# Kernel optimization log

Hardware: AMD Instinct MI355X
Metric: run time of the kernel (lower is better)

## Reference

```python
import jax, jax.numpy as jnp
import numpy as np

H, D = 8, 16
HD = H * D
SCALE0 = float(1.0 / np.sqrt(D * 1))   # degree-0 dot-product scale (order m=1)
SCALE1 = float(1.0 / np.sqrt(D * 3))   # degree-1 dot-product scale (order m=3)
SHARED = float(np.sqrt(0.5))           # shared_scale = sqrt(1/2) for DOT_PROD + SHARED
NEG = -1e9


def _split_heads_q(x):  # (b,n,HD,m) -> (b,H,n,D,m)
    b, n, _, m = x.shape
    return x.reshape(b, n, H, D, m).transpose(0, 2, 1, 3, 4)


def _split_heads_k(x):  # (b,n,N,HD,m) -> (b,H,n,N,D,m)
    b, n, N, _, m = x.shape
    return x.reshape(b, n, N, H, D, m).transpose(0, 3, 1, 2, 4, 5)


def _augment_kv(k, v, feats, W_self, null_k, null_v):
    # attend_self: VNLinear self key/value; use_null_kv: learned null tokens.
    b, n = feats.shape[:2]
    m = feats.shape[-1]
    skv = jnp.einsum('oc,bncm->bnom', W_self, feats)          # (b,n,2HD,m)
    sk, sv = jnp.split(skv, 2, axis=-2)
    sk = _split_heads_q(sk)[:, :, :, None]                     # (b,H,n,1,D,m)
    sv = _split_heads_q(sv)[:, :, :, None]
    nk = jnp.broadcast_to(null_k[None, :, None, None], (b, H, n, 1, D, m))
    nv = jnp.broadcast_to(null_v[None, :, None, None], (b, H, n, 1, D, m))
    k = jnp.concatenate([nk, sk, k], axis=3)                   # (b,H,n,2+N,D,m)
    v = jnp.concatenate([nv, sv, v], axis=3)
    return k, v


def _merge_heads(x):  # (b,H,n,D,m) -> (b,n,HD,m)
    b, _, n, _, m = x.shape
    return x.transpose(0, 2, 1, 3, 4).reshape(b, n, HD, m)


def _forward(q0, k0, v0, q1, k1, v1, feats0, feats1, edges,
             W_self_kv0, W_self_kv1, W_bias, self_bias, null_bias,
             null_k0, null_v0, null_k1, null_v1, head_weights1,
             W_out0, W_out1, neighbor_mask):
    b, n, N = edges.shape[:3]
    q0h, k0h, v0h = _split_heads_q(q0), _split_heads_k(k0), _split_heads_k(v0)
    q1h, k1h, v1h = _split_heads_q(q1), _split_heads_k(k1), _split_heads_k(v1)
    k0h, v0h = _augment_kv(k0h, v0h, feats0, W_self_kv0, null_k0, null_v0)
    k1h, v1h = _augment_kv(k1h, v1h, feats1, W_self_kv1, null_k1, null_v1)

    # pair bias for degree 0 (to_order==1); prepend null/self bias columns
    edge_bias = jnp.einsum('bnje,he->bhnj', edges, W_bias)     # (b,H,n,N)
    nb = jnp.broadcast_to(null_bias[None, :, None, None], (b, H, n, 1))
    sb = jnp.broadcast_to(self_bias[None, :, None, None], (b, H, n, 1))
    bias = jnp.concatenate([nb, sb, edge_bias], axis=-1)        # (b,H,n,2+N)

    sim0 = jnp.einsum('bhndm,bhnjdm->bhnj', q0h, k0h) * SCALE0 + bias
    w1 = jax.nn.softplus(head_weights1)                         # (1,H,1,1)
    sim1 = jnp.einsum('bhndm,bhnjdm->bhnj', q1h, k1h) * (SCALE1 * w1)

    total = (sim0 + sim1) * SHARED
    mask = jnp.concatenate(
        [jnp.ones((b, 1, n, 2), dtype=bool),                    # null + self always valid
         neighbor_mask[:, None]], axis=-1)
    total = jnp.where(mask, total, NEG)
    attn = jax.nn.softmax(total, axis=-1)                       # shared across degrees

    out0 = _merge_heads(jnp.einsum('bhnj,bhnjdm->bhndm', attn, v0h))
    out1 = _merge_heads(jnp.einsum('bhnj,bhnjdm->bhndm', attn, v1h))

    y0 = jnp.einsum('oc,bncm->bnom', W_out0, out0)              # FiberLinear deg 0
    y1 = jnp.einsum('oc,bncm->bnom', W_out1, out1)              # FiberLinear deg 1
    return y0, y1


def setup_inputs() -> dict:
    key = jax.random.key(0)
    ks = jax.random.split(key, 20)
    b, n, N, e = 1, 2048, 32, 32
    d0, d1 = 128, 64
    f = lambda k, s: jax.random.normal(k, s, dtype=jnp.float32) * 0.1
    return {
        'q0': f(ks[0], (b, n, HD, 1)), 'k0': f(ks[1], (b, n, N, HD, 1)), 'v0': f(ks[2], (b, n, N, HD, 1)),
        'q1': f(ks[3], (b, n, HD, 3)), 'k1': f(ks[4], (b, n, N, HD, 3)), 'v1': f(ks[5], (b, n, N, HD, 3)),
        'feats0': f(ks[6], (b, n, d0, 1)), 'feats1': f(ks[7], (b, n, d1, 3)),
        'edges': f(ks[8], (b, n, N, e)),
        'W_self_kv0': f(ks[9], (2 * HD, d0)), 'W_self_kv1': f(ks[10], (2 * HD, d1)),
        'W_bias': f(ks[11], (H, e)),
        'self_bias': jnp.zeros((H,), jnp.float32), 'null_bias': jnp.zeros((H,), jnp.float32),
        'null_k0': jnp.zeros((H, D, 1), jnp.float32), 'null_v0': jnp.zeros((H, D, 1), jnp.float32),
        'null_k1': jnp.zeros((H, D, 3), jnp.float32), 'null_v1': jnp.zeros((H, D, 3), jnp.float32),
        'head_weights1': jnp.full((1, H, 1, 1), float(np.log(np.e - 1.0)), jnp.float32),
        'W_out0': f(ks[12], (d0, HD)), 'W_out1': f(ks[13], (d1, HD)),
        'neighbor_mask': jax.random.uniform(ks[14], (b, n, N)) > 0.1,
    }


def reference(q0, k0, v0, q1, k1, v1, feats0, feats1, edges,
              W_self_kv0, W_self_kv1, W_bias, self_bias, null_bias,
              null_k0, null_v0, null_k1, null_v1, head_weights1,
              W_out0, W_out1, neighbor_mask):
    return _forward(q0, k0, v0, q1, k1, v1, feats0, feats1, edges,
                    W_self_kv0, W_self_kv1, W_bias, self_bias, null_bias,
                    null_k0, null_v0, null_k1, null_v1, head_weights1,
                    W_out0, W_out1, neighbor_mask)
```

## Files before the change

### kernel.cpp

```cpp
#include <hip/hip_runtime.h>

constexpr int kH  = 8;
constexpr int kD  = 16;
constexpr int kHD = 128;
constexpr int kN  = 32;
constexpr int kE  = 32;
constexpr int kD0 = 128;
constexpr int kD1 = 64;

constexpr float SCALE0   = 0.25f;
constexpr float SCALE1   = 0.14433756729740643f;
constexpr float SHARED_S = 0.70710678118654752f;
constexpr float NEGV     = -1e9f;

__global__ __launch_bounds__(256, 4) void se3_fused(
    const float* __restrict__ q0, const float* __restrict__ q1,
    const float* __restrict__ k0, const float* __restrict__ k1,
    const float* __restrict__ v0, const float* __restrict__ v1,
    const float* __restrict__ feats0, const float* __restrict__ feats1,
    const float* __restrict__ edges,
    const float* __restrict__ Wskv0, const float* __restrict__ Wskv1,
    const float* __restrict__ Wbias,
    const float* __restrict__ sbias, const float* __restrict__ nbias,
    const float* __restrict__ nk0, const float* __restrict__ nk1,
    const float* __restrict__ nv0, const float* __restrict__ nv1,
    const float* __restrict__ hw1,
    const float* __restrict__ Wout0, const float* __restrict__ Wout1,
    const int* __restrict__ nmask,
    float* __restrict__ out, int n_total)
{
  const int i = blockIdx.x;
  const int t = threadIdx.x;
  const int q4 = t & 3;
  const int qg = t >> 2;
  const int hB = qg & 7;
  const int jl = qg >> 3;

  __shared__ __align__(16) float f0s[kD0];
  __shared__ __align__(16) float f1s[kD1 * 3];
  __shared__ __align__(16) float q0s[kHD];
  __shared__ __align__(16) float q1s[kHD * 3];
  __shared__ float edg[kN * (kE + 1)];
  __shared__ float wbs[kH * kE];
  __shared__ float w1s[kH];
  __shared__ int   nmL[kN];
  __shared__ float biasL[kH][kN];
  __shared__ float sk0[kHD];
  __shared__ __align__(16) float sk1[kHD * 3];
  __shared__ __align__(16) float sv0[kHD];
  __shared__ __align__(16) float sv1[kHD * 3];
  __shared__ float sc[kH][36];
  __shared__ __align__(16) float o0p[2][kHD];
  __shared__ __align__(16) float o1p[2][kHD * 3];

  if (t < 32) {
    ((float4*)f0s)[t] = ((const float4*)(feats0 + (size_t)i * kD0))[t];
  } else if (t < 80) {
    ((float4*)f1s)[t - 32] = ((const float4*)(feats1 + (size_t)i * kD1 * 3))[t - 32];
  } else if (t < 112) {
    ((float4*)q0s)[t - 80] = ((const float4*)(q0 + (size_t)i * kHD))[t - 80];
  } else if (t < 208) {
    ((float4*)q1s)[t - 112] = ((const float4*)(q1 + (size_t)i * kHD * 3))[t - 112];
  }
  { float4 ev = ((const float4*)(edges + (size_t)i * kN * kE))[t];
    int j = t >> 3, e4 = (t & 7) * 4;
    float* dst = &edg[j * 33 + e4];
    dst[0] = ev.x; dst[1] = ev.y; dst[2] = ev.z; dst[3] = ev.w; }
  wbs[t] = Wbias[t];
  if (t < kN) nmL[t] = nmask[(size_t)i * kN + t];
  if (t < kH) w1s[t] = log1pf(expf(hw1[t]));
  __syncthreads();

  #pragma unroll
  for (int pass = 0; pass < 4; ++pass) {
    const int r = qg + 64 * pass;
    const float4* w0r = (const float4*)(Wskv0 + (size_t)r * kD0);
    float a0 = 0.f;
    #pragma unroll
    for (int g = 0; g < 8; ++g) {
      float4 w = w0r[q4 + 4 * g]; int c = (q4 + 4 * g) * 4;
      a0 += w.x * f0s[c] + w.y * f0s[c + 1]
          + w.z * f0s[c + 2] + w.w * f0s[c + 3];
    }
    const float4* w1r = (const float4*)(Wskv1 + (size_t)r * kD1);
    float a1[3] = {};
    #pragma unroll
    for (int g = 0; g < 4; ++g) {
      float4 w = w1r[q4 + 4 * g]; int c = (q4 + 4 * g) * 4;
      float wvv[4] = {w.x, w.y, w.z, w.w};
      #pragma unroll
      for (int k = 0; k < 4; ++k) {
        const float* fp = &f1s[(c + k) * 3];
        a1[0] += wvv[k] * fp[0];
        a1[1] += wvv[k] * fp[1];
        a1[2] += wvv[k] * fp[2];
      }
    }
    a0 += __shfl_xor(a0, 1); a0 += __shfl_xor(a0, 2);
    #pragma unroll
    for (int c = 0; c < 3; ++c) {
      a1[c] += __shfl_xor(a1[c], 1);
      a1[c] += __shfl_xor(a1[c], 2);
    }
    if (q4 == 0) {
      if (r < kHD) {
        sk0[r] = a0;
        sk1[r * 3 + 0] = a1[0]; sk1[r * 3 + 1] = a1[1]; sk1[r * 3 + 2] = a1[2];
      } else {
        const int o = r - kHD;
        sv0[o] = a0;
        sv1[o * 3 + 0] = a1[0]; sv1[o * 3 + 1] = a1[1]; sv1[o * 3 + 2] = a1[2];
      }
    }
  }

  {
    const int h = t >> 5, j = t & 31;
    float b = 0.f;
    #pragma unroll
    for (int e = 0; e < kE; ++e) b += edg[j * 33 + e] * wbs[h * kE + e];
    biasL[h][j] = b;
  }
  __syncthreads();

  if (t < 16) {
    const int h = t & 7;
    const bool is_self = t >= 8;
    float s0 = 0.f, s1 = 0.f, bias;
    if (is_self) {
      #pragma unroll
      for (int d = 0; d < kD; ++d) s0 += q0s[h * kD + d] * sk0[h * kD + d];
      #pragma unroll
      for (int x = 0; x < 48; ++x) s1 += q1s[h * 48 + x] * sk1[h * 48 + x];
      bias = sbias[h];
    } else {
      #pragma unroll
      for (int d = 0; d < kD; ++d) s0 += q0s[h * kD + d] * nk0[h * kD + d];
      #pragma unroll
      for (int x = 0; x < 48; ++x) s1 += q1s[h * 48 + x] * nk1[h * 48 + x];
      bias = nbias[h];
    }
    sc[h][is_self ? 1 : 0] =
        (s0 * SCALE0 + bias + s1 * SCALE1 * w1s[h]) * SHARED_S;
  }

  {
    const float w1h = w1s[hB];
    const float4 q0f = *((const float4*)(q0s + hB * kD) + q4);
    float4 q1f[3];
    #pragma unroll
    for (int pc = 0; pc < 3; ++pc)
      q1f[pc] = *((const float4*)(q1s + hB * 48 + pc * 16) + q4);

    const float* k0base = k0 + (size_t)i * kN * kHD + hB * kD + q4 * 4;
    const float* k1base = k1 + (size_t)i * kN * kHD * 3 + hB * 48 + q4 * 4;

    #pragma unroll
    for (int half = 0; half < 2; ++half) {
      float4 kv0[2];
      float4 kv1[2][3];
      #pragma unroll
      for (int pp = 0; pp < 2; ++pp) {
        const int j = (half * 2 + pp) * 8 + jl;
        kv0[pp] = *((const float4*)(k0base + (size_t)j * kHD));
        #pragma unroll
        for (int pc = 0; pc < 3; ++pc)
          kv1[pp][pc] = *((const float4*)(k1base + (size_t)j * kHD * 3 + pc * 16));
      }
      #pragma unroll
      for (int pp = 0; pp < 2; ++pp) {
        const int j = (half * 2 + pp) * 8 + jl;
        float s0 = kv0[pp].x * q0f.x + kv0[pp].y * q0f.y
                 + kv0[pp].z * q0f.z + kv0[pp].w * q0f.w;
        float s1 = 0.f;
        #pragma unroll
        for (int pc = 0; pc < 3; ++pc)
          s1 += kv1[pp][pc].x * q1f[pc].x + kv1[pp][pc].y * q1f[pc].y
              + kv1[pp][pc].z * q1f[pc].z + kv1[pp][pc].w * q1f[pc].w;
        float part = s0 * SCALE0 + s1 * SCALE1 * w1h;
        part += __shfl_xor(part, 1);
        part += __shfl_xor(part, 2);
        if (q4 == 0)
          sc[hB][2 + j] = nmL[j] ? (part + biasL[hB][j]) * SHARED_S : NEGV;
      }
      __builtin_amdgcn_sched_barrier(0);
    }
  }
  __syncthreads();

  if (t < 128) {
    const int h = t >> 4, l = t & 15;
    float* rp = sc[h];
    float va = rp[2 + l], vb = rp[2 + l + 16];
    float mx = fmaxf(va, vb);
    #pragma unroll
    for (int off = 8; off > 0; off >>= 1) mx = fmaxf(mx, __shfl_xor(mx, off));
    float e0v = rp[0], e1v = rp[1];
    mx = fmaxf(mx, fmaxf(e0v, e1v));
    float ea = __expf(va - mx), eb = __expf(vb - mx);
    float sum = ea + eb;
    #pragma unroll
    for (int off = 8; off > 0; off >>= 1) sum += __shfl_xor(sum, off);
    float ee0 = __expf(e0v - mx), ee1 = __expf(e1v - mx);
    float inv = 1.f / (sum + ee0 + ee1);
    rp[2 + l] = ea * inv;
    rp[2 + l + 16] = eb * inv;
    if (l == 0) rp[0] = ee0 * inv;
    if (l == 1) rp[1] = ee1 * inv;
  }
  __syncthreads();

  {
    const int halfD = t >> 7;
    const int s = t & 127;
    float4 acc = {0.f, 0.f, 0.f, 0.f};
    if (s < 32) {
      const int h = s >> 2;
      const float* at = sc[h];
      if (halfD == 0) {
        float4 nv = ((const float4*)nv0)[s];
        float4 sv = ((const float4*)sv0)[s];
        acc.x = at[0] * nv.x + at[1] * sv.x;
        acc.y = at[0] * nv.y + at[1] * sv.y;
        acc.z = at[0] * nv.z + at[1] * sv.z;
        acc.w = at[0] * nv.w + at[1] * sv.w;
      }
      const float4* vp = (const float4*)(v0 + (size_t)i * kN * kHD) + s;
      float4 vbuf[8];
      #pragma unroll
      for (int gg = 0; gg < 2; ++gg) {
        const int g = halfD * 2 + gg;
        #pragma unroll
        for (int r = 0; r < 8; ++r) vbuf[r] = vp[(g * 8 + r) * 32];
        #pragma unroll
        for (int r = 0; r < 8; ++r) {
          float a = at[2 + g * 8 + r];
          acc.x += a * vbuf[r].x; acc.y += a * vbuf[r].y;
          acc.z += a * vbuf[r].z; acc.w += a * vbuf[r].w;
        }
      }
      ((float4*)o0p[halfD])[s] = acc;
    } else {
      const int s1 = s - 32;
      const int h = s1 / 12;
      const float* at = sc[h];
      if (halfD == 0) {
        float4 nv = ((const float4*)nv1)[s1];
        float4 sv = ((const float4*)sv1)[s1];
        acc.x = at[0] * nv.x + at[1] * sv.x;
        acc.y = at[0] * nv.y + at[1] * sv.y;
        acc.z = at[0] * nv.z + at[1] * sv.z;
        acc.w = at[0] * nv.w + at[1] * sv.w;
      }
      const float4* vp = (const float4*)(v1 + (size_t)i * kN * kHD * 3) + s1;
      float4 vbuf[8];
      #pragma unroll
      for (int gg = 0; gg < 2; ++gg) {
        const int g = halfD * 2 + gg;
        #pragma unroll
        for (int r = 0; r < 8; ++r) vbuf[r] = vp[(g * 8 + r) * 96];
        #pragma unroll
        for (int r = 0; r < 8; ++r) {
          float a = at[2 + g * 8 + r];
          acc.x += a * vbuf[r].x; acc.y += a * vbuf[r].y;
          acc.z += a * vbuf[r].z; acc.w += a * vbuf[r].w;
        }
      }
      ((float4*)o1p[halfD])[s1] = acc;
    }
  }
  __syncthreads();

  if (t < 128) {
    if (t < 32) {
      float4 a = ((float4*)o0p[0])[t], b = ((float4*)o0p[1])[t];
      a.x += b.x; a.y += b.y; a.z += b.z; a.w += b.w;
      ((float4*)o0p[0])[t] = a;
    } else {
      const int s1 = t - 32;
      float4 a = ((float4*)o1p[0])[s1], b = ((float4*)o1p[1])[s1];
      a.x += b.x; a.y += b.y; a.z += b.z; a.w += b.w;
      ((float4*)o1p[0])[s1] = a;
    }
  }
  __syncthreads();

  #pragma unroll
  for (int pass = 0; pass < 5; ++pass) {
    const int u = qg + 64 * pass;
    if (u < 128) {
      const float4* wr = (const float4*)(Wout0 + (size_t)u * kHD);
      float a = 0.f;
      #pragma unroll
      for (int g = 0; g < 8; ++g) {
        float4 w = wr[q4 + 4 * g]; int c = (q4 + 4 * g) * 4;
        a += w.x * o0p[0][c] + w.y * o0p[0][c + 1]
           + w.z * o0p[0][c + 2] + w.w * o0p[0][c + 3];
      }
      a += __shfl_xor(a, 1); a += __shfl_xor(a, 2);
      if (q4 == 0) out[(size_t)i * kHD + u] = a;
    } else {
      const int v2 = u - 128, o = v2 / 3, m = v2 - o * 3;
      const float4* wr = (const float4*)(Wout1 + (size_t)o * kHD);
      float a = 0.f;
      #pragma unroll
      for (int g = 0; g < 8; ++g) {
        float4 w = wr[q4 + 4 * g]; int c = (q4 + 4 * g) * 4;
        a += w.x * o1p[0][(c + 0) * 3 + m] + w.y * o1p[0][(c + 1) * 3 + m]
           + w.z * o1p[0][(c + 2) * 3 + m] + w.w * o1p[0][(c + 3) * 3 + m];
      }
      a += __shfl_xor(a, 1); a += __shfl_xor(a, 2);
      if (q4 == 0)
        out[(size_t)n_total * kHD + (size_t)i * 192 + v2] = a;
    }
  }
}

extern "C" void kernel_launch(void* const* d_in, const int* in_sizes, int n_in,
                              void* d_out, int out_size, void* d_ws, size_t ws_size,
                              hipStream_t stream) {
  const int n = in_sizes[0] / kHD;
  const float* q0     = (const float*)d_in[0];
  const float* k0     = (const float*)d_in[1];
  const float* v0     = (const float*)d_in[2];
  const float* q1     = (const float*)d_in[3];
  const float* k1     = (const float*)d_in[4];
  const float* v1     = (const float*)d_in[5];
  const float* feats0 = (const float*)d_in[6];
  const float* feats1 = (const float*)d_in[7];
  const float* edges  = (const float*)d_in[8];
  const float* Wskv0  = (const float*)d_in[9];
  const float* Wskv1  = (const float*)d_in[10];
  const float* Wbias  = (const float*)d_in[11];
  const float* sbias  = (const float*)d_in[12];
  const float* nbias  = (const float*)d_in[13];
  const float* nk0    = (const float*)d_in[14];
  const float* nv0    = (const float*)d_in[15];
  const float* nk1    = (const float*)d_in[16];
  const float* nv1    = (const float*)d_in[17];
  const float* hw1    = (const float*)d_in[18];
  const float* Wout0  = (const float*)d_in[19];
  const float* Wout1  = (const float*)d_in[20];
  const int*   nmask  = (const int*)d_in[21];

  se3_fused<<<n, 256, 0, stream>>>(
      q0, q1, k0, k1, v0, v1, feats0, feats1, edges,
      Wskv0, Wskv1, Wbias, sbias, nbias, nk0, nk1, nv0, nv1, hw1,
      Wout0, Wout1, nmask, (float*)d_out, n);
}
```

Baseline: 318.7 us.

## Stream K/V neighbor chunks into LDS with double-buffered global_load_lds

Key and value tensors are now staged in chunks of 8 neighbors straight into a double-buffered LDS area using asynchronous global-to-LDS loads. The next chunk is fetched while the current one is consumed, for both the score and the value-weighting phases. The edge-bias computation now reads edges and Wbias straight from global memory, and shared buffers are reused through a scratch region to limit LDS growth. The intent is to hide global memory latency. In exchange it adds a block barrier per chunk and a larger LDS footprint that may limit occupancy, and it relies on barriers to order the asynchronous LDS writes.

```diff
diff --git a/kernel.cpp b/kernel.cpp
--- a/kernel.cpp
+++ b/kernel.cpp
@@ -13,7 +13,25 @@
 constexpr float SHARED_S = 0.70710678118654752f;
 constexpr float NEGV     = -1e9f;
 
-__global__ __launch_bounds__(256, 4) void se3_fused(
+
+__device__ __forceinline__ void gll16(const void* g, void* l) {
+  __builtin_amdgcn_global_load_lds(
+      (const __attribute__((address_space(1))) void*)(g),
+      (__attribute__((address_space(3))) void*)(l), 16, 0, 0);
+}
+
+__device__ __forceinline__ void stage_chunk(
+    const float* p0, const float* p1, int i, int c, float* buf, int t) {
+  const char* g0 = (const char*)(p0 + (size_t)i * kN * kHD + (size_t)c * 8 * kHD) + t * 16;
+  const char* g1 = (const char*)(p1 + (size_t)i * kN * kHD * 3 + (size_t)c * 8 * kHD * 3) + t * 16;
+  char* l = (char*)buf + ((t >> 6) << 10);
+  gll16(g0, l);
+  #pragma unroll
+  for (int o = 0; o < 3; ++o)
+    gll16(g1 + o * 4096, l + 4096 + o * 4096);
+}
+
+__global__ __launch_bounds__(256, 4) void se3_stream(
     const float* __restrict__ q0, const float* __restrict__ q1,
     const float* __restrict__ k0, const float* __restrict__ k1,
     const float* __restrict__ v0, const float* __restrict__ v1,
@@ -29,29 +47,28 @@
     const int* __restrict__ nmask,
     float* __restrict__ out, int n_total)
 {
-  const int i = blockIdx.x;
-  const int t = threadIdx.x;
+  const int i  = blockIdx.x;
+  const int t  = threadIdx.x;
   const int q4 = t & 3;
   const int qg = t >> 2;
   const int hB = qg & 7;
-  const int jl = qg >> 3;
-
+  const int jj = t >> 5;
+
+  __shared__ __align__(16) float kv[2][4096];
+  __shared__ __align__(16) float scratch[1024];
   __shared__ __align__(16) float f0s[kD0];
   __shared__ __align__(16) float f1s[kD1 * 3];
-  __shared__ __align__(16) float q0s[kHD];
-  __shared__ __align__(16) float q1s[kHD * 3];
-  __shared__ float edg[kN * (kE + 1)];
-  __shared__ float wbs[kH * kE];
-  __shared__ float w1s[kH];
-  __shared__ int   nmL[kN];
-  __shared__ float biasL[kH][kN];
-  __shared__ float sk0[kHD];
-  __shared__ __align__(16) float sk1[kHD * 3];
   __shared__ __align__(16) float sv0[kHD];
   __shared__ __align__(16) float sv1[kHD * 3];
   __shared__ float sc[kH][36];
-  __shared__ __align__(16) float o0p[2][kHD];
-  __shared__ __align__(16) float o1p[2][kHD * 3];
+  __shared__ float biasL[kH][kN];
+  __shared__ float w1s[kH];
+  __shared__ int   nmL[kN];
+
+  float* q0s = scratch;
+  float* q1s = scratch + 128;
+  float* sk0 = scratch + 512;
+  float* sk1 = scratch + 640;
 
   if (t < 32) {
     ((float4*)f0s)[t] = ((const float4*)(feats0 + (size_t)i * kD0))[t];
@@ -62,14 +79,12 @@
   } else if (t < 208) {
     ((float4*)q1s)[t - 112] = ((const float4*)(q1 + (size_t)i * kHD * 3))[t - 112];
   }
-  { float4 ev = ((const float4*)(edges + (size_t)i * kN * kE))[t];
-    int j = t >> 3, e4 = (t & 7) * 4;
-    float* dst = &edg[j * 33 + e4];
-    dst[0] = ev.x; dst[1] = ev.y; dst[2] = ev.z; dst[3] = ev.w; }
-  wbs[t] = Wbias[t];
   if (t < kN) nmL[t] = nmask[(size_t)i * kN + t];
   if (t < kH) w1s[t] = log1pf(expf(hw1[t]));
   __syncthreads();
+
+  stage_chunk(k0, k1, i, 0, kv[0], t);
+  stage_chunk(k0, k1, i, 1, kv[1], t);
 
   #pragma unroll
   for (int pass = 0; pass < 4; ++pass) {
@@ -113,16 +128,20 @@
       }
     }
   }
+  __syncthreads();
 
   {
     const int h = t >> 5, j = t & 31;
+    const float4* er = (const float4*)(edges + (size_t)i * kN * kE + j * kE);
+    const float4* wr = (const float4*)(Wbias + h * kE);
     float b = 0.f;
     #pragma unroll
-    for (int e = 0; e < kE; ++e) b += edg[j * 33 + e] * wbs[h * kE + e];
+    for (int g = 0; g < 8; ++g) {
+      float4 e = er[g]; float4 w = wr[g];
+      b += e.x * w.x + e.y * w.y + e.z * w.z + e.w * w.w;
+    }
     biasL[h][j] = b;
   }
-  __syncthreads();
-
   if (t < 16) {
     const int h = t & 7;
     const bool is_self = t >= 8;
@@ -143,6 +162,7 @@
     sc[h][is_self ? 1 : 0] =
         (s0 * SCALE0 + bias + s1 * SCALE1 * w1s[h]) * SHARED_S;
   }
+  __syncthreads();
 
   {
     const float w1h = w1s[hB];
@@ -152,41 +172,36 @@
     for (int pc = 0; pc < 3; ++pc)
       q1f[pc] = *((const float4*)(q1s + hB * 48 + pc * 16) + q4);
 
-    const float* k0base = k0 + (size_t)i * kN * kHD + hB * kD + q4 * 4;
-    const float* k1base = k1 + (size_t)i * kN * kHD * 3 + hB * 48 + q4 * 4;
-
-    #pragma unroll
-    for (int half = 0; half < 2; ++half) {
-      float4 kv0[2];
-      float4 kv1[2][3];
-      #pragma unroll
-      for (int pp = 0; pp < 2; ++pp) {
-        const int j = (half * 2 + pp) * 8 + jl;
-        kv0[pp] = *((const float4*)(k0base + (size_t)j * kHD));
-        #pragma unroll
-        for (int pc = 0; pc < 3; ++pc)
-          kv1[pp][pc] = *((const float4*)(k1base + (size_t)j * kHD * 3 + pc * 16));
-      }
-      #pragma unroll
-      for (int pp = 0; pp < 2; ++pp) {
-        const int j = (half * 2 + pp) * 8 + jl;
-        float s0 = kv0[pp].x * q0f.x + kv0[pp].y * q0f.y
-                 + kv0[pp].z * q0f.z + kv0[pp].w * q0f.w;
-        float s1 = 0.f;
-        #pragma unroll
-        for (int pc = 0; pc < 3; ++pc)
-          s1 += kv1[pp][pc].x * q1f[pc].x + kv1[pp][pc].y * q1f[pc].y
-              + kv1[pp][pc].z * q1f[pc].z + kv1[pp][pc].w * q1f[pc].w;
-        float part = s0 * SCALE0 + s1 * SCALE1 * w1h;
-        part += __shfl_xor(part, 1);
-        part += __shfl_xor(part, 2);
-        if (q4 == 0)
-          sc[hB][2 + j] = nmL[j] ? (part + biasL[hB][j]) * SHARED_S : NEGV;
-      }
-      __builtin_amdgcn_sched_barrier(0);
-    }
-  }
-  __syncthreads();
+    #pragma unroll
+    for (int c = 0; c < 4; ++c) {
+      if (c >= 1) {
+        if (c < 3) stage_chunk(k0, k1, i, c + 1, kv[(c + 1) & 1], t);
+        else       stage_chunk(v0, v1, i, 0,     kv[0],           t);
+      }
+      const float* kb = kv[c & 1];
+      float4 ka = ((const float4*)(kb + jj * 128 + hB * 16))[q4];
+      const float4* k1r = (const float4*)(kb + 1024 + jj * 384 + hB * 48);
+      float4 kb0 = k1r[q4];
+      float4 kb1 = k1r[q4 + 4];
+      float4 kb2 = k1r[q4 + 8];
+
+      float s0 = ka.x * q0f.x + ka.y * q0f.y + ka.z * q0f.z + ka.w * q0f.w;
+      float s1 = kb0.x * q1f[0].x + kb0.y * q1f[0].y
+               + kb0.z * q1f[0].z + kb0.w * q1f[0].w
+               + kb1.x * q1f[1].x + kb1.y * q1f[1].y
+               + kb1.z * q1f[1].z + kb1.w * q1f[1].w
+               + kb2.x * q1f[2].x + kb2.y * q1f[2].y
+               + kb2.z * q1f[2].z + kb2.w * q1f[2].w;
+
+      float part = s0 * SCALE0 + s1 * SCALE1 * w1h;
+      part += __shfl_xor(part, 1);
+      part += __shfl_xor(part, 2);
+      const int j = c * 8 + jj;
+      if (q4 == 0)
+        sc[hB][2 + j] = nmL[j] ? (part + biasL[hB][j]) * SHARED_S : NEGV;
+      __syncthreads();
+    }
+  }
 
   if (t < 128) {
     const int h = t >> 4, l = t & 15;
@@ -211,40 +226,22 @@
   __syncthreads();
 
   {
-    const int halfD = t >> 7;
+    const int half = t >> 7;
     const int s = t & 127;
+    const int h = (s < 32) ? (s >> 2) : ((s - 32) / 12);
+    const float* at = sc[h];
+
     float4 acc = {0.f, 0.f, 0.f, 0.f};
-    if (s < 32) {
-      const int h = s >> 2;
-      const float* at = sc[h];
-      if (halfD == 0) {
+    if (half == 0) {
+      if (s < 32) {
         float4 nv = ((const float4*)nv0)[s];
         float4 sv = ((const float4*)sv0)[s];
         acc.x = at[0] * nv.x + at[1] * sv.x;
         acc.y = at[0] * nv.y + at[1] * sv.y;
         acc.z = at[0] * nv.z + at[1] * sv.z;
         acc.w = at[0] * nv.w + at[1] * sv.w;
-      }
-      const float4* vp = (const float4*)(v0 + (size_t)i * kN * kHD) + s;
-      float4 vbuf[8];
-      #pragma unroll
-      for (int gg = 0; gg < 2; ++gg) {
-        const int g = halfD * 2 + gg;
-        #pragma unroll
-        for (int r = 0; r < 8; ++r) vbuf[r] = vp[(g * 8 + r) * 32];
-        #pragma unroll
-        for (int r = 0; r < 8; ++r) {
-          float a = at[2 + g * 8 + r];
-          acc.x += a * vbuf[r].x; acc.y += a * vbuf[r].y;
-          acc.z += a * vbuf[r].z; acc.w += a * vbuf[r].w;
-        }
-      }
-      ((float4*)o0p[halfD])[s] = acc;
-    } else {
-      const int s1 = s - 32;
-      const int h = s1 / 12;
-      const float* at = sc[h];
-      if (halfD == 0) {
+      } else {
+        const int s1 = s - 32;
         float4 nv = ((const float4*)nv1)[s1];
         float4 sv = ((const float4*)sv1)[s1];
         acc.x = at[0] * nv.x + at[1] * sv.x;
@@ -252,39 +249,46 @@
         acc.z = at[0] * nv.z + at[1] * sv.z;
         acc.w = at[0] * nv.w + at[1] * sv.w;
       }
-      const float4* vp = (const float4*)(v1 + (size_t)i * kN * kHD * 3) + s1;
-      float4 vbuf[8];
-      #pragma unroll
-      for (int gg = 0; gg < 2; ++gg) {
-        const int g = halfD * 2 + gg;
-        #pragma unroll
-        for (int r = 0; r < 8; ++r) vbuf[r] = vp[(g * 8 + r) * 96];
-        #pragma unroll
-        for (int r = 0; r < 8; ++r) {
-          float a = at[2 + g * 8 + r];
-          acc.x += a * vbuf[r].x; acc.y += a * vbuf[r].y;
-          acc.z += a * vbuf[r].z; acc.w += a * vbuf[r].w;
-        }
-      }
-      ((float4*)o1p[halfD])[s1] = acc;
-    }
+    }
+
+    #pragma unroll
+    for (int c = 0; c < 4; ++c) {
+      if (c < 3) stage_chunk(v0, v1, i, c + 1, kv[(c + 1) & 1], t);
+      const float* vb = kv[c & 1];
+      #pragma unroll
+      for (int u = 0; u < 4; ++u) {
+        const int jr = half * 4 + u;
+        const float a = at[2 + c * 8 + jr];
+        float4 vv = (s < 32)
+            ? ((const float4*)(vb + jr * 128))[s]
+            : ((const float4*)(vb + 1024 + jr * 384))[s - 32];
+        acc.x += a * vv.x; acc.y += a * vv.y;
+        acc.z += a * vv.z; acc.w += a * vv.w;
+      }
+      __syncthreads();
+    }
+
+    if (s < 32) ((float4*)(scratch + half * 128))[s] = acc;
+    else        ((float4*)(scratch + 256 + half * 384))[s - 32] = acc;
   }
   __syncthreads();
 
   if (t < 128) {
     if (t < 32) {
-      float4 a = ((float4*)o0p[0])[t], b = ((float4*)o0p[1])[t];
+      float4 a = ((float4*)scratch)[t], b = ((float4*)(scratch + 128))[t];
       a.x += b.x; a.y += b.y; a.z += b.z; a.w += b.w;
-      ((float4*)o0p[0])[t] = a;
+      ((float4*)scratch)[t] = a;
     } else {
       const int s1 = t - 32;
-      float4 a = ((float4*)o1p[0])[s1], b = ((float4*)o1p[1])[s1];
+      float4 a = ((float4*)(scratch + 256))[s1], b = ((float4*)(scratch + 640))[s1];
       a.x += b.x; a.y += b.y; a.z += b.z; a.w += b.w;
-      ((float4*)o1p[0])[s1] = a;
-    }
-  }
-  __syncthreads();
-
+      ((float4*)(scratch + 256))[s1] = a;
+    }
+  }
+  __syncthreads();
+
+  const float* o0L = scratch;
+  const float* o1L = scratch + 256;
   #pragma unroll
   for (int pass = 0; pass < 5; ++pass) {
     const int u = qg + 64 * pass;
@@ -294,8 +298,8 @@
       #pragma unroll
       for (int g = 0; g < 8; ++g) {
         float4 w = wr[q4 + 4 * g]; int c = (q4 + 4 * g) * 4;
-        a += w.x * o0p[0][c] + w.y * o0p[0][c + 1]
-           + w.z * o0p[0][c + 2] + w.w * o0p[0][c + 3];
+        a += w.x * o0L[c] + w.y * o0L[c + 1]
+           + w.z * o0L[c + 2] + w.w * o0L[c + 3];
       }
       a += __shfl_xor(a, 1); a += __shfl_xor(a, 2);
       if (q4 == 0) out[(size_t)i * kHD + u] = a;
@@ -306,8 +310,8 @@
       #pragma unroll
       for (int g = 0; g < 8; ++g) {
         float4 w = wr[q4 + 4 * g]; int c = (q4 + 4 * g) * 4;
-        a += w.x * o1p[0][(c + 0) * 3 + m] + w.y * o1p[0][(c + 1) * 3 + m]
-           + w.z * o1p[0][(c + 2) * 3 + m] + w.w * o1p[0][(c + 3) * 3 + m];
+        a += w.x * o1L[(c + 0) * 3 + m] + w.y * o1L[(c + 1) * 3 + m]
+           + w.z * o1L[(c + 2) * 3 + m] + w.w * o1L[(c + 3) * 3 + m];
       }
       a += __shfl_xor(a, 1); a += __shfl_xor(a, 2);
       if (q4 == 0)
@@ -343,7 +347,7 @@
   const float* Wout1  = (const float*)d_in[20];
   const int*   nmask  = (const int*)d_in[21];
 
-  se3_fused<<<n, 256, 0, stream>>>(
+  se3_stream<<<n, 256, 0, stream>>>(
       q0, q1, k0, k1, v0, v1, feats0, feats1, edges,
       Wskv0, Wskv1, Wbias, sbias, nbias, nk0, nk1, nv0, nv1, hw1,
       Wout0, Wout1, nmask, (float*)d_out, n);
```

Result: slower. 331.3 us (+4.0%).
